# Kernel tuning notes

Measured on AMD Instinct MI355X. Metric: run time of the kernel, lower is better.

## Reference

```python
import jax, jax.numpy as jnp
import numpy as np

B, S, D, H = 8, 1024, 1024, 16
DH = D // H
LN_EPS = 1e-5
SLOPE = 0.01  # nn.LeakyReLU default negative_slope


def _ln(x, g, b):
    m = x.mean(-1, keepdims=True)
    v = ((x - m) ** 2).mean(-1, keepdims=True)
    return (x - m) / jnp.sqrt(v + LN_EPS) * g + b


def _leaky(x):
    return jnp.where(x >= 0, x, SLOPE * x)


def setup_inputs() -> dict:
    key = jax.random.key(0)
    ks = jax.random.split(key, 6)
    q = jax.random.normal(ks[0], (B, S, D), dtype=jnp.float32)
    masks = jnp.ones((B, S), dtype=jnp.int32)  # all-valid mask (masked_fill is a no-op)
    w1 = jax.random.normal(ks[1], (D, D), dtype=jnp.float32) * 0.02
    b1 = jnp.zeros((D,), jnp.float32)
    w2 = jax.random.normal(ks[2], (D, D), dtype=jnp.float32) * 0.02
    b2 = jnp.zeros((D,), jnp.float32)
    ones = jnp.ones((D,), jnp.float32)
    zeros = jnp.zeros((D,), jnp.float32)
    return dict(q=q, masks=masks,
                w1=w1, b1=b1, ln1_g=ones, ln1_b=zeros,
                w2=w2, b2=b2, ln2_g=ones, ln2_b=zeros,
                anf_g=ones, anf_b=zeros,
                an1_g=ones, an1_b=zeros,
                an2_g=ones, an2_b=zeros)


def reference(q, masks, w1, b1, ln1_g, ln1_b, w2, b2, ln2_g, ln2_b,
              anf_g, anf_b, an1_g, an1_b, an2_g, an2_b):
    # --- multi-head cosine-similarity attention (k = v = q, no projections) ---
    qh = q.reshape(B, S, H, DH).transpose(0, 2, 1, 3)  # (B,H,S,DH) == separate_heads
    qn = qh / jnp.clip(jnp.linalg.norm(qh, axis=-1, keepdims=True), 1e-8)
    # cosine similarity scores, softmax over keys
    w = jax.nn.softmax(jnp.einsum('bhqd,bhkd->bhqk', qn, qn), axis=-1)
    # masked_fill AFTER softmax (faithful to source: mask per (batch, query))
    w = jnp.where(masks[:, None, :, None] == 0, jnp.float32(-1e9), w)
    heads = jnp.einsum('bhqk,bhkd->bhqd', w, qh)
    attn = heads.transpose(0, 2, 1, 3).reshape(B, S, D)  # concat_heads
    # --- add_norm1 (dropout=0.5 but eval mode => identity) ---
    y1 = _ln(q + attn, an1_g, an1_b)
    # --- PositionWiseFFN: Linear->LN->LeakyReLU x2, then internal AddNorm ---
    h = _leaky(_ln(y1 @ w1 + b1, ln1_g, ln1_b))
    y = _leaky(_ln(h @ w2 + b2, ln2_g, ln2_b))
    y2 = _ln(y1 + y, anf_g, anf_b)
    # --- add_norm2 ---
    return _ln(y1 + y2, an2_g, an2_b)
```

## Files before the change

kernel.cpp:

```cpp
#include <hip/hip_runtime.h>
#include <hip/hip_bf16.h>

#define BB 8
#define SS 1024
#define DD 1024
#define HH 16

typedef __attribute__((ext_vector_type(8))) short short8;
typedef __attribute__((ext_vector_type(8))) __bf16 bf16x8;
typedef __attribute__((ext_vector_type(4))) float f32x4;

__device__ inline float bf2f(unsigned short h){
  unsigned u = ((unsigned)h) << 16;
  return __builtin_bit_cast(float, u);
}
__device__ inline unsigned short f2bf(float f){
  unsigned u = __builtin_bit_cast(unsigned, f);
  u += 0x7fffu + ((u >> 16) & 1u);
  return (unsigned short)(u >> 16);
}
__device__ inline f32x4 mfma16(short8 a, short8 b, f32x4 c){
  return __builtin_amdgcn_mfma_f32_16x16x32_bf16(
      __builtin_bit_cast(bf16x8, a), __builtin_bit_cast(bf16x8, b), c, 0, 0, 0);
}
__device__ inline void gld_lds16(const unsigned short* g, unsigned short* l){
  __builtin_amdgcn_global_load_lds((const __attribute__((address_space(1))) void*)g,
      (__attribute__((address_space(3))) void*)l, 16, 0, 0);
}

__global__ __launch_bounds__(256) void prep_w(const float* __restrict__ w1,
                                              const float* __restrict__ w2,
                                              unsigned short* __restrict__ w1T,
                                              unsigned short* __restrict__ w2T){
  __shared__ float tile[64][65];
  const float* src = blockIdx.z ? w2 : w1;
  unsigned short* dst = blockIdx.z ? w2T : w1T;
  int k0 = blockIdx.x * 64, n0 = blockIdx.y * 64;
  int tx = threadIdx.x & 63, ty = threadIdx.x >> 6;
#pragma unroll
  for (int r = 0; r < 16; ++r)
    tile[ty + 4*r][tx] = src[(k0 + ty + 4*r) * DD + n0 + tx];
  __syncthreads();
#pragma unroll
  for (int r = 0; r < 16; ++r)
    dst[(n0 + ty + 4*r) * DD + k0 + tx] = f2bf(tile[tx][ty + 4*r]);
}

__global__ __launch_bounds__(256) void prep_q(const float* __restrict__ q,
                                              unsigned short* __restrict__ kf,
                                              unsigned short* __restrict__ vf,
                                              unsigned short* __restrict__ qb){
  __shared__ float tile[64][65];
  __shared__ float rinv[64];
  int bh = blockIdx.x >> 4, st = blockIdx.x & 15;
  int b = bh >> 4, h = bh & 15;
  int t = threadIdx.x;
  int tx = t & 63, ty = t >> 6;
  int srow = b * SS + st * 64;
#pragma unroll
  for (int r = 0; r < 16; ++r)
    tile[ty + 4*r][tx] = q[(size_t)(srow + ty + 4*r) * DD + h * 64 + tx];
  __syncthreads();
  {
    int s = t >> 2, p = t & 3;
    float ssum = 0.f;
#pragma unroll
    for (int i = 0; i < 16; ++i){ float v = tile[s][p*16 + i]; ssum += v * v; }
    ssum += __shfl_xor(ssum, 1);
    ssum += __shfl_xor(ssum, 2);
    if (p == 0) rinv[s] = 1.0f / fmaxf(sqrtf(ssum), 1e-8f);
  }
  __syncthreads();
#pragma unroll
  for (int r = 0; r < 16; ++r)
    qb[(size_t)(srow + ty + 4*r) * DD + h * 64 + tx] = f2bf(tile[ty + 4*r][tx]);
#pragma unroll
  for (int v = 0; v < 2; ++v){
    int idx = t * 2 + v;
    int c_l = idx >> 6, lane = idx & 63;
    int g2 = c_l >> 2, c = (c_l >> 1) & 1, hf = c_l & 1;
    int lrq = lane & 15, lgq = lane >> 4;
    int s = g2 * 32 + (lrq >> 2) * 8 + c * 4 + (lrq & 3);
    int d0 = hf * 32 + lgq * 8;
    float rv = rinv[s];
    short8 o;
#pragma unroll
    for (int e = 0; e < 8; ++e) o[e] = (short)f2bf(tile[s][d0 + e] * rv);
    *(short8*)(kf + ((size_t)(bh * 128 + st * 8 + c_l) * 64 + lane) * 8) = o;
  }
#pragma unroll
  for (int v = 0; v < 2; ++v){
    int idx = t * 2 + v;
    int kt2 = idx >> 8, db = (idx >> 6) & 3, lane = idx & 63;
    int d = db * 16 + (lane & 15);
    int k0 = kt2 * 32 + (lane >> 4) * 8;
    short8 o;
#pragma unroll
    for (int e = 0; e < 8; ++e) o[e] = (short)f2bf(tile[k0 + e][d]);
    *(short8*)(vf + ((size_t)((bh * 32 + st * 2 + kt2) * 4 + db) * 512 + lane * 8)) = o;
  }
}

__global__ __launch_bounds__(512, 6) void attn_kern(const unsigned short* __restrict__ kf,
                                                    const unsigned short* __restrict__ vf,
                                                    const int* __restrict__ masks,
                                                    unsigned short* __restrict__ attnb){
  __shared__ unsigned short Kb[2][4][64 * 8];
  __shared__ unsigned short Vb[2][4][64 * 8];
  __shared__ int anym;
  const int bh = blockIdx.x, b = bh >> 4, h = bh & 15;
  const int by = blockIdx.y;
  const int t = threadIdx.x, w = t >> 6, l = t & 63;
  const int lr = l & 15, lg = l >> 4;
  if (t == 0) anym = 0;
  __syncthreads();
  if (t < 128 && masks[b * SS + by * 128 + t] == 0) anym = 1;

  short8 aQ[2];
#pragma unroll
  for (int hf = 0; hf < 2; ++hf)
    aQ[hf] = *(const short8*)(kf +
        ((size_t)(bh * 128 + by * 16 + (w >> 1) * 4 + (w & 1) * 2 + hf) * 64 + l) * 8);

  if (w < 4){
    gld_lds16(kf + ((size_t)(bh * 128 + w) * 64 + l) * 8, &Kb[0][w][0]);
  } else {
    gld_lds16(vf + ((size_t)((bh * 32 + 0) * 4 + (w - 4)) * 512 + l * 8), &Vb[0][w - 4][0]);
  }
  __syncthreads();

  f32x4 o[4] = {};
  float rs0 = 0.f, rs1 = 0.f;

  for (int it = 0; it < 32; ++it){
    const int cur = it & 1, nxt = cur ^ 1;
    if (it + 1 < 32){
      if (w < 4)
        gld_lds16(kf + ((size_t)(bh * 128 + (it + 1) * 4 + w) * 64 + l) * 8, &Kb[nxt][w][0]);
      else
        gld_lds16(vf + ((size_t)((bh * 32 + it + 1) * 4 + (w - 4)) * 512 + l * 8), &Vb[nxt][w - 4][0]);
    }
    f32x4 sc[2];
#pragma unroll
    for (int c = 0; c < 2; ++c){
      short8 a0 = *(const short8*)&Kb[cur][c * 2 + 0][l * 8];
      short8 a1 = *(const short8*)&Kb[cur][c * 2 + 1][l * 8];
      f32x4 z = {0.f, 0.f, 0.f, 0.f};
      z = mfma16(a0, aQ[0], z);
      z = mfma16(a1, aQ[1], z);
      sc[c] = z;
    }
    bf16x8 pav;
#pragma unroll
    for (int c = 0; c < 2; ++c)
#pragma unroll
      for (int j = 0; j < 4; ++j){
        float pv = __expf(sc[c][j] - 1.0f);
        if (j & 1) rs1 += pv; else rs0 += pv;
        pav[c * 4 + j] = (__bf16)pv;
      }
    short8 pa = __builtin_bit_cast(short8, pav);
#pragma unroll
    for (int db = 0; db < 4; ++db){
      short8 bV = *(const short8*)&Vb[cur][db][l * 8];
      o[db] = mfma16(pa, bV, o[db]);
    }
    __syncthreads();
  }

  float rsum = rs0 + rs1;
  rsum += __shfl_xor(rsum, 16);
  rsum += __shfl_xor(rsum, 32);
  float inv = 1.0f / rsum;
  float invj[4];
#pragma unroll
  for (int j = 0; j < 4; ++j) invj[j] = __shfl(inv, lg * 4 + j);

#pragma unroll
  for (int db = 0; db < 4; ++db)
#pragma unroll
    for (int j = 0; j < 4; ++j){
      int qrow = by * 128 + (w >> 1) * 32 + lg * 8 + (w & 1) * 4 + j;
      float val = o[db][j] * invj[j];
      if (anym && masks[b * SS + qrow] == 0){
        float vs = 0.f;
        for (int kt = 0; kt < 32; ++kt)
          for (int lgp = 0; lgp < 4; ++lgp){
            const unsigned short* vp = vf +
                ((size_t)((bh * 32 + kt) * 4 + db) * 512 + (lgp * 16 + lr) * 8);
            for (int e = 0; e < 8; ++e) vs += bf2f(vp[e]);
          }
        val = -1e9f * vs;
      }
      attnb[(size_t)(b * SS + qrow) * DD + h * 64 + db * 16 + lr] = f2bf(val);
    }
}

__device__ inline float2 block_reduce2(float a, float bq){
  __shared__ float sm[8];
#pragma unroll
  for (int off = 1; off < 64; off <<= 1){
    a += __shfl_xor(a, off);
    bq += __shfl_xor(bq, off);
  }
  int w = threadIdx.x >> 6;
  if ((threadIdx.x & 63) == 0){ sm[2*w] = a; sm[2*w + 1] = bq; }
  __syncthreads();
  float2 r;
  r.x = sm[0] + sm[2] + sm[4] + sm[6];
  r.y = sm[1] + sm[3] + sm[5] + sm[7];
  __syncthreads();
  return r;
}

__global__ __launch_bounds__(256) void addnorm1(const unsigned short* __restrict__ qb,
                                                const unsigned short* __restrict__ attnb,
                                                const float* __restrict__ g,
                                                const float* __restrict__ bt,
                                                unsigned short* __restrict__ y1b){
  int row = blockIdx.x, t = threadIdx.x;
  ushort4 qv = *(const ushort4*)(qb + (size_t)row * DD + t * 4);
  ushort4 av = *(const ushort4*)(attnb + (size_t)row * DD + t * 4);
  float x[4] = { bf2f(qv.x) + bf2f(av.x), bf2f(qv.y) + bf2f(av.y),
                 bf2f(qv.z) + bf2f(av.z), bf2f(qv.w) + bf2f(av.w) };
  float s = 0.f, ssq = 0.f;
#pragma unroll
  for (int i = 0; i < 4; ++i){ s += x[i]; ssq += x[i] * x[i]; }
  float2 r = block_reduce2(s, ssq);
  float m = r.x * (1.0f / DD);
  float rs = rsqrtf(r.y * (1.0f / DD) - m * m + 1e-5f);
  float4 gv = *(const float4*)(g + t * 4);
  float4 bv = *(const float4*)(bt + t * 4);
  float y[4] = { (x[0]-m)*rs*gv.x + bv.x, (x[1]-m)*rs*gv.y + bv.y,
                 (x[2]-m)*rs*gv.z + bv.z, (x[3]-m)*rs*gv.w + bv.w };
  ushort4 ob = { f2bf(y[0]), f2bf(y[1]), f2bf(y[2]), f2bf(y[3]) };
  *(ushort4*)(y1b + (size_t)row * DD + t * 4) = ob;
}

__global__ __launch_bounds__(256, 2) void gemm_bias(const unsigned short* __restrict__ X,
                                                    const unsigned short* __restrict__ WT,
                                                    const float* __restrict__ bias,
                                                    unsigned short* __restrict__ out){
  __shared__ unsigned short As[128 * 32];
  __shared__ unsigned short Bs[128 * 32];
  int t = threadIdx.x, l = t & 63, w = t >> 6;
  int wm = w >> 1, wn = w & 1;
  int lr = l & 15, lg = l >> 4;
  int bm = blockIdx.x * 128, bn = blockIdx.y * 128;
  f32x4 acc[4][4] = {};
  int r = t >> 2, cb = (t & 3) * 8;
  for (int kt = 0; kt < 32; ++kt){
    __syncthreads();
    {
      const unsigned short* ga0 = X  + (size_t)(bm +      r) * 1024 + kt * 32 + cb;
      const unsigned short* ga1 = X  + (size_t)(bm + 64 + r) * 1024 + kt * 32 + cb;
      const unsigned short* gb0 = WT + (size_t)(bn +      r) * 1024 + kt * 32 + cb;
      const unsigned short* gb1 = WT + (size_t)(bn + 64 + r) * 1024 + kt * 32 + cb;
      __builtin_amdgcn_global_load_lds((const __attribute__((address_space(1))) void*)ga0,
          (__attribute__((address_space(3))) void*)((char*)As + w * 1024), 16, 0, 0);
      __builtin_amdgcn_global_load_lds((const __attribute__((address_space(1))) void*)ga1,
          (__attribute__((address_space(3))) void*)((char*)As + 4096 + w * 1024), 16, 0, 0);
      __builtin_amdgcn_global_load_lds((const __attribute__((address_space(1))) void*)gb0,
          (__attribute__((address_space(3))) void*)((char*)Bs + w * 1024), 16, 0, 0);
      __builtin_amdgcn_global_load_lds((const __attribute__((address_space(1))) void*)gb1,
          (__attribute__((address_space(3))) void*)((char*)Bs + 4096 + w * 1024), 16, 0, 0);
    }
    __syncthreads();
    short8 aA[4], bB[4];
#pragma unroll
    for (int i = 0; i < 4; ++i)
      aA[i] = *(const short8*)&As[(wm * 64 + i * 16 + lr) * 32 + lg * 8];
#pragma unroll
    for (int i = 0; i < 4; ++i)
      bB[i] = *(const short8*)&Bs[(wn * 64 + i * 16 + lr) * 32 + lg * 8];
#pragma unroll
    for (int mi = 0; mi < 4; ++mi)
#pragma unroll
      for (int ni = 0; ni < 4; ++ni)
        acc[mi][ni] = mfma16(aA[mi], bB[ni], acc[mi][ni]);
  }
#pragma unroll
  for (int ni = 0; ni < 4; ++ni){
    int col = bn + wn * 64 + ni * 16 + lr;
    float bv = bias[col];
#pragma unroll
    for (int mi = 0; mi < 4; ++mi){
      int row0 = bm + wm * 64 + mi * 16 + lg * 4;
#pragma unroll
      for (int j = 0; j < 4; ++j)
        out[(size_t)(row0 + j) * 1024 + col] = f2bf(acc[mi][ni][j] + bv);
    }
  }
}

__global__ __launch_bounds__(256) void ln_leaky(const unsigned short* __restrict__ in,
                                                const float* __restrict__ g,
                                                const float* __restrict__ bt,
                                                unsigned short* __restrict__ out){
  int row = blockIdx.x, t = threadIdx.x;
  ushort4 iv = *(const ushort4*)(in + (size_t)row * DD + t * 4);
  float x[4] = { bf2f(iv.x), bf2f(iv.y), bf2f(iv.z), bf2f(iv.w) };
  float s = 0.f, ssq = 0.f;
#pragma unroll
  for (int i = 0; i < 4; ++i){ s += x[i]; ssq += x[i] * x[i]; }
  float2 r = block_reduce2(s, ssq);
  float m = r.x * (1.0f / DD);
  float rs = rsqrtf(r.y * (1.0f / DD) - m * m + 1e-5f);
  float4 gv = *(const float4*)(g + t * 4);
  float4 bv = *(const float4*)(bt + t * 4);
  ushort4 ov;
  {
    float v0 = (x[0]-m)*rs*gv.x + bv.x; v0 = v0 >= 0.f ? v0 : 0.01f*v0; ov.x = f2bf(v0);
    float v1 = (x[1]-m)*rs*gv.y + bv.y; v1 = v1 >= 0.f ? v1 : 0.01f*v1; ov.y = f2bf(v1);
    float v2 = (x[2]-m)*rs*gv.z + bv.z; v2 = v2 >= 0.f ? v2 : 0.01f*v2; ov.z = f2bf(v2);
    float v3 = (x[3]-m)*rs*gv.w + bv.w; v3 = v3 >= 0.f ? v3 : 0.01f*v3; ov.w = f2bf(v3);
  }
  *(ushort4*)(out + (size_t)row * DD + t * 4) = ov;
}

__global__ __launch_bounds__(256) void final_kern(const unsigned short* __restrict__ g2,
                                                  const unsigned short* __restrict__ y1,
                                                  const float* __restrict__ ln2g, const float* __restrict__ ln2b,
                                                  const float* __restrict__ anfg, const float* __restrict__ anfb,
                                                  const float* __restrict__ an2g, const float* __restrict__ an2b,
                                                  float* __restrict__ out){
  int row = blockIdx.x, t = threadIdx.x;
  ushort4 iv = *(const ushort4*)(g2 + (size_t)row * DD + t * 4);
  ushort4 y1v = *(const ushort4*)(y1 + (size_t)row * DD + t * 4);
  float x[4] = { bf2f(iv.x), bf2f(iv.y), bf2f(iv.z), bf2f(iv.w) };
  float yy1[4] = { bf2f(y1v.x), bf2f(y1v.y), bf2f(y1v.z), bf2f(y1v.w) };
  float s = 0.f, ssq = 0.f;
#pragma unroll
  for (int i = 0; i < 4; ++i){ s += x[i]; ssq += x[i]*x[i]; }
  float2 r = block_reduce2(s, ssq);
  float m = r.x * (1.0f / DD);
  float rs = rsqrtf(r.y * (1.0f / DD) - m*m + 1e-5f);
  float4 gv = *(const float4*)(ln2g + t * 4);
  float4 bv = *(const float4*)(ln2b + t * 4);
  float y[4] = { (x[0]-m)*rs*gv.x + bv.x, (x[1]-m)*rs*gv.y + bv.y,
                 (x[2]-m)*rs*gv.z + bv.z, (x[3]-m)*rs*gv.w + bv.w };
#pragma unroll
  for (int i = 0; i < 4; ++i) y[i] = y[i] >= 0.f ? y[i] : 0.01f*y[i];

  float tv[4]; s = 0.f; ssq = 0.f;
#pragma unroll
  for (int i = 0; i < 4; ++i){ tv[i] = yy1[i] + y[i]; s += tv[i]; ssq += tv[i]*tv[i]; }
  r = block_reduce2(s, ssq);
  m = r.x * (1.0f / DD);
  rs = rsqrtf(r.y * (1.0f / DD) - m*m + 1e-5f);
  gv = *(const float4*)(anfg + t * 4);
  bv = *(const float4*)(anfb + t * 4);
  float y2[4] = { (tv[0]-m)*rs*gv.x + bv.x, (tv[1]-m)*rs*gv.y + bv.y,
                  (tv[2]-m)*rs*gv.z + bv.z, (tv[3]-m)*rs*gv.w + bv.w };

  float u[4]; s = 0.f; ssq = 0.f;
#pragma unroll
  for (int i = 0; i < 4; ++i){ u[i] = yy1[i] + y2[i]; s += u[i]; ssq += u[i]*u[i]; }
  r = block_reduce2(s, ssq);
  m = r.x * (1.0f / DD);
  rs = rsqrtf(r.y * (1.0f / DD) - m*m + 1e-5f);
  gv = *(const float4*)(an2g + t * 4);
  bv = *(const float4*)(an2b + t * 4);
  float4 ov = { (u[0]-m)*rs*gv.x + bv.x, (u[1]-m)*rs*gv.y + bv.y,
                (u[2]-m)*rs*gv.z + bv.z, (u[3]-m)*rs*gv.w + bv.w };
  *(float4*)(out + (size_t)row * DD + t * 4) = ov;
}

extern "C" void kernel_launch(void* const* d_in, const int* in_sizes, int n_in,
                              void* d_out, int out_size, void* d_ws, size_t ws_size,
                              hipStream_t stream){
  const float* q    = (const float*)d_in[0];
  const int* masks  = (const int*)d_in[1];
  const float* w1   = (const float*)d_in[2];
  const float* b1   = (const float*)d_in[3];
  const float* ln1g = (const float*)d_in[4];
  const float* ln1b = (const float*)d_in[5];
  const float* w2   = (const float*)d_in[6];
  const float* b2   = (const float*)d_in[7];
  const float* ln2g = (const float*)d_in[8];
  const float* ln2b = (const float*)d_in[9];
  const float* anfg = (const float*)d_in[10];
  const float* anfb = (const float*)d_in[11];
  const float* an1g = (const float*)d_in[12];
  const float* an1b = (const float*)d_in[13];
  const float* an2g = (const float*)d_in[14];
  const float* an2b = (const float*)d_in[15];

  char* ws = (char*)d_ws;
  unsigned short* w1T  = (unsigned short*)(ws + 0);
  unsigned short* w2T  = (unsigned short*)(ws + 2097152);
  unsigned short* kf   = (unsigned short*)(ws + 4194304);
  unsigned short* vf   = (unsigned short*)(ws + 20971520);
  unsigned short* attn = (unsigned short*)(ws + 37748736);
  unsigned short* y1b  = (unsigned short*)(ws + 54525952);
  unsigned short* qb   = (unsigned short*)(ws + 71303168);
  unsigned short* g1   = kf;
  unsigned short* hbuf = vf;
  unsigned short* g2   = attn;
  float* outp = (float*)d_out;

  prep_w<<<dim3(16, 16, 2), 256, 0, stream>>>(w1, w2, w1T, w2T);
  prep_q<<<dim3(2048), 256, 0, stream>>>(q, kf, vf, qb);
  attn_kern<<<dim3(128, 8), 512, 0, stream>>>(kf, vf, masks, attn);
  addnorm1<<<dim3(8192), 256, 0, stream>>>(qb, attn, an1g, an1b, y1b);
  gemm_bias<<<dim3(64, 8), 256, 0, stream>>>(y1b, w1T, b1, g1);
  ln_leaky<<<dim3(8192), 256, 0, stream>>>(g1, ln1g, ln1b, hbuf);
  gemm_bias<<<dim3(64, 8), 256, 0, stream>>>(hbuf, w2T, b2, g2);
  final_kern<<<dim3(8192), 256, 0, stream>>>(g2, y1b, ln2g, ln2b, anfg, anfb, an2g, an2b, outp);
}
```

Measured before the change: 162.9 us.

## Deepen attention K/V prefetch to a four-stage ring with explicit waitcnt barriers

The attention kernel's double-buffered K/V loads into LDS become a 4-slot ring buffer with three tiles in flight. The per-iteration __syncthreads is replaced by explicit vmcnt/lgkmcnt waits plus s_barrier, so outstanding global loads can stay in flight. Launch bounds rise for the attention kernel (6 to 8 waves) and the GEMM (2 to 3 blocks). The aim is to hide global memory latency better, at the cost of doubled LDS use and tighter register limits that could cause spills.

```diff
diff --git a/kernel.cpp b/kernel.cpp
--- a/kernel.cpp
+++ b/kernel.cpp
@@ -101,12 +101,13 @@
   }
 }
 
-__global__ __launch_bounds__(512, 6) void attn_kern(const unsigned short* __restrict__ kf,
+#define NT 32
+__global__ __launch_bounds__(512, 8) void attn_kern(const unsigned short* __restrict__ kf,
                                                     const unsigned short* __restrict__ vf,
                                                     const int* __restrict__ masks,
                                                     unsigned short* __restrict__ attnb){
-  __shared__ unsigned short Kb[2][4][64 * 8];
-  __shared__ unsigned short Vb[2][4][64 * 8];
+  __shared__ unsigned short Kb[4][4][64 * 8];
+  __shared__ unsigned short Vb[4][4][64 * 8];
   __shared__ int anym;
   const int bh = blockIdx.x, b = bh >> 4, h = bh & 15;
   const int by = blockIdx.y;
@@ -115,6 +116,7 @@
   if (t == 0) anym = 0;
   __syncthreads();
   if (t < 128 && masks[b * SS + by * 128 + t] == 0) anym = 1;
+  __syncthreads();
 
   short8 aQ[2];
 #pragma unroll
@@ -122,23 +124,27 @@
     aQ[hf] = *(const short8*)(kf +
         ((size_t)(bh * 128 + by * 16 + (w >> 1) * 4 + (w & 1) * 2 + hf) * 64 + l) * 8);
 
-  if (w < 4){
-    gld_lds16(kf + ((size_t)(bh * 128 + w) * 64 + l) * 8, &Kb[0][w][0]);
-  } else {
-    gld_lds16(vf + ((size_t)((bh * 32 + 0) * 4 + (w - 4)) * 512 + l * 8), &Vb[0][w - 4][0]);
-  }
-  __syncthreads();
+#pragma unroll
+  for (int p = 0; p < 3; ++p){
+    if (w < 4)
+      gld_lds16(kf + ((size_t)(bh * 128 + p * 4 + w) * 64 + l) * 8, &Kb[p][w][0]);
+    else
+      gld_lds16(vf + ((size_t)((bh * 32 + p) * 4 + (w - 4)) * 512 + l * 8), &Vb[p][w - 4][0]);
+  }
+  asm volatile("s_waitcnt vmcnt(2)" ::: "memory");
+  __builtin_amdgcn_s_barrier();
 
   f32x4 o[4] = {};
   float rs0 = 0.f, rs1 = 0.f;
 
-  for (int it = 0; it < 32; ++it){
-    const int cur = it & 1, nxt = cur ^ 1;
-    if (it + 1 < 32){
+  for (int it = 0; it < NT; ++it){
+    const int cur = it & 3;
+    if (it + 3 < NT){
+      const int nb = (it + 3) & 3;
       if (w < 4)
-        gld_lds16(kf + ((size_t)(bh * 128 + (it + 1) * 4 + w) * 64 + l) * 8, &Kb[nxt][w][0]);
+        gld_lds16(kf + ((size_t)(bh * 128 + (it + 3) * 4 + w) * 64 + l) * 8, &Kb[nb][w][0]);
       else
-        gld_lds16(vf + ((size_t)((bh * 32 + it + 1) * 4 + (w - 4)) * 512 + l * 8), &Vb[nxt][w - 4][0]);
+        gld_lds16(vf + ((size_t)((bh * 32 + it + 3) * 4 + (w - 4)) * 512 + l * 8), &Vb[nb][w - 4][0]);
     }
     f32x4 sc[2];
 #pragma unroll
@@ -165,7 +171,13 @@
       short8 bV = *(const short8*)&Vb[cur][db][l * 8];
       o[db] = mfma16(pa, bV, o[db]);
     }
-    __syncthreads();
+    if (it + 1 < NT){
+      asm volatile("s_waitcnt lgkmcnt(0)" ::: "memory");
+      if (it + 3 < NT)      asm volatile("s_waitcnt vmcnt(2)" ::: "memory");
+      else if (it + 2 < NT) asm volatile("s_waitcnt vmcnt(1)" ::: "memory");
+      else                  asm volatile("s_waitcnt vmcnt(0)" ::: "memory");
+      __builtin_amdgcn_s_barrier();
+    }
   }
 
   float rsum = rs0 + rs1;
@@ -237,7 +249,7 @@
   *(ushort4*)(y1b + (size_t)row * DD + t * 4) = ob;
 }
 
-__global__ __launch_bounds__(256, 2) void gemm_bias(const unsigned short* __restrict__ X,
+__global__ __launch_bounds__(256, 3) void gemm_bias(const unsigned short* __restrict__ X,
                                                     const unsigned short* __restrict__ WT,
                                                     const float* __restrict__ bias,
                                                     unsigned short* __restrict__ out){
```

Measured after the change: 167.4 us. +2.8%, slower.

## Triple-buffer attention and GEMM loads, double query rows per attention block

Applied to the files above, without the earlier changes.

The attention kernel now gives each wave two query chunks, so each block covers 256 queries and each K/V tile loaded into LDS is reused twice as often. Its main loop moves to 3-stage buffering with two K/V tiles per phase and explicit vmcnt waits. The GEMM also switches to a 3-stage async global-to-LDS pipeline with a single barrier per k-step instead of two syncthreads. Together these aim to hide load latency and cut barrier and global traffic. In exchange they use more LDS and registers, halve the attention grid, and reduce occupancy.

```diff
diff --git a/kernel.cpp b/kernel.cpp
--- a/kernel.cpp
+++ b/kernel.cpp
@@ -101,12 +101,13 @@
   }
 }
 
-__global__ __launch_bounds__(512, 6) void attn_kern(const unsigned short* __restrict__ kf,
+#define NPH 16
+__global__ __launch_bounds__(512, 4) void attn_kern(const unsigned short* __restrict__ kf,
                                                     const unsigned short* __restrict__ vf,
                                                     const int* __restrict__ masks,
                                                     unsigned short* __restrict__ attnb){
-  __shared__ unsigned short Kb[2][4][64 * 8];
-  __shared__ unsigned short Vb[2][4][64 * 8];
+  __shared__ unsigned short Kb[3][8][512];
+  __shared__ unsigned short Vb[3][8][512];
   __shared__ int anym;
   const int bh = blockIdx.x, b = bh >> 4, h = bh & 15;
   const int by = blockIdx.y;
@@ -114,86 +115,120 @@
   const int lr = l & 15, lg = l >> 4;
   if (t == 0) anym = 0;
   __syncthreads();
-  if (t < 128 && masks[b * SS + by * 128 + t] == 0) anym = 1;
-
-  short8 aQ[2];
-#pragma unroll
-  for (int hf = 0; hf < 2; ++hf)
-    aQ[hf] = *(const short8*)(kf +
-        ((size_t)(bh * 128 + by * 16 + (w >> 1) * 4 + (w & 1) * 2 + hf) * 64 + l) * 8);
-
-  if (w < 4){
-    gld_lds16(kf + ((size_t)(bh * 128 + w) * 64 + l) * 8, &Kb[0][w][0]);
-  } else {
-    gld_lds16(vf + ((size_t)((bh * 32 + 0) * 4 + (w - 4)) * 512 + l * 8), &Vb[0][w - 4][0]);
-  }
-  __syncthreads();
-
-  f32x4 o[4] = {};
-  float rs0 = 0.f, rs1 = 0.f;
-
-  for (int it = 0; it < 32; ++it){
-    const int cur = it & 1, nxt = cur ^ 1;
-    if (it + 1 < 32){
-      if (w < 4)
-        gld_lds16(kf + ((size_t)(bh * 128 + (it + 1) * 4 + w) * 64 + l) * 8, &Kb[nxt][w][0]);
-      else
-        gld_lds16(vf + ((size_t)((bh * 32 + it + 1) * 4 + (w - 4)) * 512 + l * 8), &Vb[nxt][w - 4][0]);
+  if (t < 256 && masks[b * SS + by * 256 + t] == 0) anym = 1;
+
+  short8 aQ[2][2];
+#pragma unroll
+  for (int c = 0; c < 2; ++c)
+#pragma unroll
+    for (int hf = 0; hf < 2; ++hf)
+      aQ[c][hf] = *(const short8*)(kf +
+          ((size_t)(bh * 128 + (by * 8 + w) * 4 + c * 2 + hf) * 64 + l) * 8);
+
+#define STAGE(ph, bf) do {                                                            \
+    if (w < 4){                                                                       \
+      gld_lds16(kf + ((size_t)(bh * 128 + (2*(ph)) * 4 + w) * 64 + l) * 8,            \
+                &Kb[bf][w][0]);                                                       \
+      gld_lds16(kf + ((size_t)(bh * 128 + (2*(ph)+1) * 4 + w) * 64 + l) * 8,          \
+                &Kb[bf][4 + w][0]);                                                   \
+    } else {                                                                          \
+      gld_lds16(vf + ((size_t)((bh * 32 + 2*(ph)) * 4 + (w - 4)) * 512 + l * 8),      \
+                &Vb[bf][w - 4][0]);                                                   \
+      gld_lds16(vf + ((size_t)((bh * 32 + 2*(ph)+1) * 4 + (w - 4)) * 512 + l * 8),    \
+                &Vb[bf][4 + (w - 4)][0]);                                             \
+    }                                                                                 \
+  } while (0)
+
+  STAGE(0, 0);
+  STAGE(1, 1);
+  asm volatile("s_waitcnt vmcnt(2) lgkmcnt(0)" ::: "memory");
+  __builtin_amdgcn_s_barrier();
+
+  f32x4 o[2][4] = {};
+  float rsum[2] = {0.f, 0.f};
+
+  for (int ph = 0; ph < NPH; ++ph){
+    const int cur = ph % 3;
+    if (ph + 2 < NPH) STAGE(ph + 2, (ph + 2) % 3);
+#pragma unroll
+    for (int gi = 0; gi < 2; ++gi){
+      short8 bK[2][2];
+#pragma unroll
+      for (int c = 0; c < 2; ++c)
+#pragma unroll
+        for (int hf = 0; hf < 2; ++hf)
+          bK[c][hf] = *(const short8*)&Kb[cur][gi * 4 + c * 2 + hf][l * 8];
+      f32x4 sc[2][2];
+#pragma unroll
+      for (int qc = 0; qc < 2; ++qc)
+#pragma unroll
+        for (int c = 0; c < 2; ++c){
+          f32x4 z = {0.f, 0.f, 0.f, 0.f};
+          z = mfma16(bK[c][0], aQ[qc][0], z);
+          z = mfma16(bK[c][1], aQ[qc][1], z);
+          sc[qc][c] = z;
+        }
+      bf16x8 pav[2];
+#pragma unroll
+      for (int qc = 0; qc < 2; ++qc)
+#pragma unroll
+        for (int c = 0; c < 2; ++c)
+#pragma unroll
+          for (int j = 0; j < 4; ++j){
+            float pv = __expf(sc[qc][c][j] - 1.0f);
+            rsum[qc] += pv;
+            pav[qc][c * 4 + j] = (__bf16)pv;
+          }
+      short8 pa0 = __builtin_bit_cast(short8, pav[0]);
+      short8 pa1 = __builtin_bit_cast(short8, pav[1]);
+#pragma unroll
+      for (int db = 0; db < 4; ++db){
+        short8 bV = *(const short8*)&Vb[cur][gi * 4 + db][l * 8];
+        o[0][db] = mfma16(pa0, bV, o[0][db]);
+        o[1][db] = mfma16(pa1, bV, o[1][db]);
+      }
     }
-    f32x4 sc[2];
-#pragma unroll
-    for (int c = 0; c < 2; ++c){
-      short8 a0 = *(const short8*)&Kb[cur][c * 2 + 0][l * 8];
-      short8 a1 = *(const short8*)&Kb[cur][c * 2 + 1][l * 8];
-      f32x4 z = {0.f, 0.f, 0.f, 0.f};
-      z = mfma16(a0, aQ[0], z);
-      z = mfma16(a1, aQ[1], z);
-      sc[c] = z;
+    if (ph + 1 < NPH){
+      asm volatile("s_waitcnt lgkmcnt(0)" ::: "memory");
+      if (ph + 2 < NPH) asm volatile("s_waitcnt vmcnt(2)" ::: "memory");
+      else              asm volatile("s_waitcnt vmcnt(0)" ::: "memory");
+      __builtin_amdgcn_s_barrier();
     }
-    bf16x8 pav;
-#pragma unroll
-    for (int c = 0; c < 2; ++c)
+  }
+
+  float invq[2];
+#pragma unroll
+  for (int qc = 0; qc < 2; ++qc){
+    float r = rsum[qc];
+    r += __shfl_xor(r, 16);
+    r += __shfl_xor(r, 32);
+    invq[qc] = 1.0f / r;
+  }
+#pragma unroll
+  for (int qc = 0; qc < 2; ++qc){
+    float invj[4];
+#pragma unroll
+    for (int j = 0; j < 4; ++j) invj[j] = __shfl(invq[qc], lg * 4 + j);
+#pragma unroll
+    for (int db = 0; db < 4; ++db)
 #pragma unroll
       for (int j = 0; j < 4; ++j){
-        float pv = __expf(sc[c][j] - 1.0f);
-        if (j & 1) rs1 += pv; else rs0 += pv;
-        pav[c * 4 + j] = (__bf16)pv;
+        int qrow = by * 256 + w * 32 + lg * 8 + qc * 4 + j;
+        float val = o[qc][db][j] * invj[j];
+        if (anym && masks[b * SS + qrow] == 0){
+          float vs = 0.f;
+          for (int kt = 0; kt < 32; ++kt)
+            for (int lgp = 0; lgp < 4; ++lgp){
+              const unsigned short* vp = vf +
+                  ((size_t)((bh * 32 + kt) * 4 + db) * 512 + (lgp * 16 + lr) * 8);
+              for (int e = 0; e < 8; ++e) vs += bf2f(vp[e]);
+            }
+          val = -1e9f * vs;
+        }
+        attnb[(size_t)(b * SS + qrow) * DD + h * 64 + db * 16 + lr] = f2bf(val);
       }
-    short8 pa = __builtin_bit_cast(short8, pav);
-#pragma unroll
-    for (int db = 0; db < 4; ++db){
-      short8 bV = *(const short8*)&Vb[cur][db][l * 8];
-      o[db] = mfma16(pa, bV, o[db]);
-    }
-    __syncthreads();
-  }
-
-  float rsum = rs0 + rs1;
-  rsum += __shfl_xor(rsum, 16);
-  rsum += __shfl_xor(rsum, 32);
-  float inv = 1.0f / rsum;
-  float invj[4];
-#pragma unroll
-  for (int j = 0; j < 4; ++j) invj[j] = __shfl(inv, lg * 4 + j);
-
-#pragma unroll
-  for (int db = 0; db < 4; ++db)
-#pragma unroll
-    for (int j = 0; j < 4; ++j){
-      int qrow = by * 128 + (w >> 1) * 32 + lg * 8 + (w & 1) * 4 + j;
-      float val = o[db][j] * invj[j];
-      if (anym && masks[b * SS + qrow] == 0){
-        float vs = 0.f;
-        for (int kt = 0; kt < 32; ++kt)
-          for (int lgp = 0; lgp < 4; ++lgp){
-            const unsigned short* vp = vf +
-                ((size_t)((bh * 32 + kt) * 4 + db) * 512 + (lgp * 16 + lr) * 8);
-            for (int e = 0; e < 8; ++e) vs += bf2f(vp[e]);
-          }
-        val = -1e9f * vs;
-      }
-      attnb[(size_t)(b * SS + qrow) * DD + h * 64 + db * 16 + lr] = f2bf(val);
-    }
+  }
+#undef STAGE
 }
 
 __device__ inline float2 block_reduce2(float a, float bq){
@@ -241,44 +276,54 @@
                                                     const unsigned short* __restrict__ WT,
                                                     const float* __restrict__ bias,
                                                     unsigned short* __restrict__ out){
-  __shared__ unsigned short As[128 * 32];
-  __shared__ unsigned short Bs[128 * 32];
+  __shared__ unsigned short As[3][128 * 32];
+  __shared__ unsigned short Bs[3][128 * 32];
   int t = threadIdx.x, l = t & 63, w = t >> 6;
   int wm = w >> 1, wn = w & 1;
   int lr = l & 15, lg = l >> 4;
   int bm = blockIdx.x * 128, bn = blockIdx.y * 128;
   f32x4 acc[4][4] = {};
   int r = t >> 2, cb = (t & 3) * 8;
+
+#define GSTAGE(kt, bf) do {                                                        \
+    gld_lds16(X  + (size_t)(bm +      r) * 1024 + (kt) * 32 + cb,                  \
+              &As[bf][w * 512]);                                                   \
+    gld_lds16(X  + (size_t)(bm + 64 + r) * 1024 + (kt) * 32 + cb,                  \
+              &As[bf][2048 + w * 512]);                                            \
+    gld_lds16(WT + (size_t)(bn +      r) * 1024 + (kt) * 32 + cb,                  \
+              &Bs[bf][w * 512]);                                                   \
+    gld_lds16(WT + (size_t)(bn + 64 + r) * 1024 + (kt) * 32 + cb,                  \
+              &Bs[bf][2048 + w * 512]);                                            \
+  } while (0)
+
+  GSTAGE(0, 0);
+  GSTAGE(1, 1);
+  asm volatile("s_waitcnt vmcnt(4)" ::: "memory");
+  __builtin_amdgcn_s_barrier();
+
   for (int kt = 0; kt < 32; ++kt){
-    __syncthreads();
-    {
-      const unsigned short* ga0 = X  + (size_t)(bm +      r) * 1024 + kt * 32 + cb;
-      const unsigned short* ga1 = X  + (size_t)(bm + 64 + r) * 1024 + kt * 32 + cb;
-      const unsigned short* gb0 = WT + (size_t)(bn +      r) * 1024 + kt * 32 + cb;
-      const unsigned short* gb1 = WT + (size_t)(bn + 64 + r) * 1024 + kt * 32 + cb;
-      __builtin_amdgcn_global_load_lds((const __attribute__((address_space(1))) void*)ga0,
-          (__attribute__((address_space(3))) void*)((char*)As + w * 1024), 16, 0, 0);
-      __builtin_amdgcn_global_load_lds((const __attribute__((address_space(1))) void*)ga1,
-          (__attribute__((address_space(3))) void*)((char*)As + 4096 + w * 1024), 16, 0, 0);
-      __builtin_amdgcn_global_load_lds((const __attribute__((address_space(1))) void*)gb0,
-          (__attribute__((address_space(3))) void*)((char*)Bs + w * 1024), 16, 0, 0);
-      __builtin_amdgcn_global_load_lds((const __attribute__((address_space(1))) void*)gb1,
-          (__attribute__((address_space(3))) void*)((char*)Bs + 4096 + w * 1024), 16, 0, 0);
-    }
-    __syncthreads();
+    const int cur = kt % 3;
+    if (kt + 2 < 32) GSTAGE(kt + 2, (kt + 2) % 3);
     short8 aA[4], bB[4];
 #pragma unroll
     for (int i = 0; i < 4; ++i)
-      aA[i] = *(const short8*)&As[(wm * 64 + i * 16 + lr) * 32 + lg * 8];
+      aA[i] = *(const short8*)&As[cur][(wm * 64 + i * 16 + lr) * 32 + lg * 8];
 #pragma unroll
     for (int i = 0; i < 4; ++i)
-      bB[i] = *(const short8*)&Bs[(wn * 64 + i * 16 + lr) * 32 + lg * 8];
+      bB[i] = *(const short8*)&Bs[cur][(wn * 64 + i * 16 + lr) * 32 + lg * 8];
 #pragma unroll
     for (int mi = 0; mi < 4; ++mi)
 #pragma unroll
       for (int ni = 0; ni < 4; ++ni)
         acc[mi][ni] = mfma16(aA[mi], bB[ni], acc[mi][ni]);
-  }
+    if (kt + 1 < 32){
+      asm volatile("s_waitcnt lgkmcnt(0)" ::: "memory");
+      if (kt + 2 < 32) asm volatile("s_waitcnt vmcnt(4)" ::: "memory");
+      else             asm volatile("s_waitcnt vmcnt(0)" ::: "memory");
+      __builtin_amdgcn_s_barrier();
+    }
+  }
+#undef GSTAGE
 #pragma unroll
   for (int ni = 0; ni < 4; ++ni){
     int col = bn + wn * 64 + ni * 16 + lr;
@@ -401,7 +446,7 @@
 
   prep_w<<<dim3(16, 16, 2), 256, 0, stream>>>(w1, w2, w1T, w2T);
   prep_q<<<dim3(2048), 256, 0, stream>>>(q, kf, vf, qb);
-  attn_kern<<<dim3(128, 8), 512, 0, stream>>>(kf, vf, masks, attn);
+  attn_kern<<<dim3(128, 4), 512, 0, stream>>>(kf, vf, masks, attn);
   addnorm1<<<dim3(8192), 256, 0, stream>>>(qb, attn, an1g, an1b, y1b);
   gemm_bias<<<dim3(64, 8), 256, 0, stream>>>(y1b, w1T, b1, g1);
   ln_leaky<<<dim3(8192), 256, 0, stream>>>(g1, ln1g, ln1b, hbuf);
```

Measured after the change: 158.1 us. 2.9% less time.
